# Kernel tuning notes

Measured on AMD Instinct MI355X. Metric: run time of the kernel, lower is better.

## Reference

```python
import jax, jax.numpy as jnp
import numpy as np

N_NODES = 100000
N_EDGES = 3200000
D_IN = 256
D_OUT = 256


def setup_inputs() -> dict:
    key = jax.random.key(0)
    k1, k2, k3, k4, k5 = jax.random.split(key, 5)
    x = jax.random.normal(k1, (N_NODES, D_IN), dtype=jnp.float32)
    # xavier-uniform-like init for weight
    limit = float(np.sqrt(6.0 / (D_IN + D_OUT)))
    weight = jax.random.uniform(k2, (D_IN, D_OUT), dtype=jnp.float32, minval=-limit, maxval=limit)
    edge_val = jax.random.uniform(k3, (N_EDGES,), dtype=jnp.float32)
    edge_row = jax.random.randint(k4, (N_EDGES,), 0, N_NODES, dtype=jnp.int32)
    edge_col = jax.random.randint(k5, (N_EDGES,), 0, N_NODES, dtype=jnp.int32)
    return {"x": x, "weight": weight, "edge_val": edge_val,
            "edge_row": edge_row, "edge_col": edge_col}


def reference(x, weight, edge_val, edge_row, edge_col):
    # dropout p=0.0 -> identity
    support = x @ weight                                  # [N, D_OUT]
    # spmm: out[r] += val * support[c] for each edge (r, c, val)
    msgs = support[edge_col] * edge_val[:, None]          # [E, D_OUT]
    out = jax.ops.segment_sum(msgs, edge_row, num_segments=N_NODES)
    return jax.nn.relu(out)
```

## Files before the change

### kernel.cpp

```cpp
#include <hip/hip_runtime.h>

#define N_NODES 100000
#define N_EDGES 3200000
#define D 256
#define OVF_MAX 8192

#define RPB 256
#define NBUCK 391
#define CAPB 11264

#define CHUNK 4096
#define NBLK_A ((N_EDGES + CHUNK - 1) / CHUNK)

#define GEMM_BLOCKS (N_NODES / 16)
#define SCAP 9216

typedef __attribute__((ext_vector_type(8))) short bf16x8;
typedef __attribute__((ext_vector_type(4))) float f32x4;
typedef __attribute__((ext_vector_type(2))) float f32x2;

__device__ unsigned short g_wtp[(size_t)16 * 8 * 64 * 8];
__device__ unsigned short g_support[(size_t)N_NODES * D];
__device__ int   g_bucket_cur[NBUCK];
__device__ int2  g_binned[(size_t)NBUCK * CAPB];
__device__ int   g_novf;
__device__ int   g_ovf_row[OVF_MAX];
__device__ int2  g_ovf_edge[OVF_MAX];

__device__ __forceinline__ unsigned short f2bf(float f) {
    unsigned u = __float_as_uint(f);
    unsigned r = u + 0x7fffu + ((u >> 16) & 1u);
    return (unsigned short)(r >> 16);
}

__global__ void setup_kernel(const float* __restrict__ W) {
    const int tid = threadIdx.x;
    if (blockIdx.x < 64) {
        int pb = (blockIdx.x * 256 + tid) * 4;
        #pragma unroll
        for (int j = 0; j < 4; ++j) {
            int p    = pb + j;
            int i8   = p & 7;
            int lane = (p >> 3) & 63;
            int s    = (p >> 9) & 7;
            int nt   = p >> 12;
            int n = nt * 16 + (lane & 15);
            int k = s * 32 + (lane >> 4) * 8 + i8;
            g_wtp[p] = f2bf(W[(size_t)k * D + n]);
        }
    }
    for (int i = blockIdx.x * blockDim.x + tid; i < NBUCK;
         i += gridDim.x * blockDim.x)
        g_bucket_cur[i] = 0;
    if (blockIdx.x == 0 && tid == 0) g_novf = 0;
}

union SmemK2 {
    struct {
        int2 rec[CHUNK];
        int  cnt[NBUCK];
        int  pre[NBUCK + 1];
        int  bas[NBUCK];
    } bin;
    float tile[4][16][68];
};

__launch_bounds__(256)
__global__ void bin_gemm_kernel(const float* __restrict__ x,
                                const float* __restrict__ edge_val,
                                const int* __restrict__ edge_row,
                                const int* __restrict__ edge_col) {
    __shared__ SmemK2 sm;
    const int tid = threadIdx.x;
    const int b = blockIdx.x;

    if (b < NBLK_A) {
        auto& B = sm.bin;
        const int e0 = b * CHUNK;
        for (int q = tid; q < NBUCK; q += 256) B.cnt[q] = 0;
        __syncthreads();
        #pragma unroll
        for (int j = 0; j < CHUNK / 256; ++j) {
            int e = e0 + tid + j * 256;
            if (e < N_EDGES) atomicAdd(&B.cnt[edge_row[e] >> 8], 1);
        }
        __syncthreads();
        if (tid == 0) {
            int run = 0;
            for (int q = 0; q < NBUCK; ++q) { B.pre[q] = run; run += B.cnt[q]; }
            B.pre[NBUCK] = run;
        }
        __syncthreads();
        for (int q = tid; q < NBUCK; q += 256)
            B.bas[q] = B.cnt[q] ? atomicAdd(&g_bucket_cur[q], B.cnt[q]) : 0;
        __syncthreads();
        for (int q = tid; q < NBUCK; q += 256) B.cnt[q] = 0;
        __syncthreads();
        #pragma unroll
        for (int j = 0; j < CHUNK / 256; ++j) {
            int e = e0 + tid + j * 256;
            if (e < N_EDGES) {
                int r = edge_row[e];
                int q = r >> 8;
                int o = atomicAdd(&B.cnt[q], 1);
                int2 pk;
                pk.x = edge_col[e] | ((r & 255) << 17);
                pk.y = __float_as_int(edge_val[e]);
                B.rec[B.pre[q] + o] = pk;
            }
        }
        __syncthreads();
        const int total = B.pre[NBUCK];
        for (int i = tid; i < total; i += 256) {
            int lo = 0, hi = NBUCK;
            while (hi - lo > 1) {
                int mid = (lo + hi) >> 1;
                if (B.pre[mid] <= i) lo = mid; else hi = mid;
            }
            int q = lo;
            int dest = B.bas[q] + (i - B.pre[q]);
            int2 pk = B.rec[i];
            if (dest < CAPB) {
                g_binned[(size_t)q * CAPB + dest] = pk;
            } else {
                int o = atomicAdd(&g_novf, 1);
                if (o < OVF_MAX) {
                    g_ovf_row[o] = (q << 8) | (pk.x >> 17);
                    int2 ov; ov.x = pk.x & 0x1FFFF; ov.y = pk.y;
                    g_ovf_edge[o] = ov;
                }
            }
        }
    } else {
        const int g    = b - NBLK_A;
        const int wave = tid >> 6;
        const int lane = tid & 63;
        const int m0   = g * 16;
        const int n0   = wave * 64;
        const int lm   = lane & 15;
        const int q    = lane >> 4;

        f32x4 acc0 = {}, acc1 = {}, acc2 = {}, acc3 = {};

        #pragma unroll
        for (int s = 0; s < 8; ++s) {
            const int k0 = s * 32;
            const float* Arow = &x[(size_t)(m0 + lm) * D + k0 + q * 8];
            float4 f0 = *(const float4*)&Arow[0];
            float4 f1 = *(const float4*)&Arow[4];
            union { bf16x8 v; unsigned short u[8]; } au;
            au.u[0] = f2bf(f0.x); au.u[1] = f2bf(f0.y);
            au.u[2] = f2bf(f0.z); au.u[3] = f2bf(f0.w);
            au.u[4] = f2bf(f1.x); au.u[5] = f2bf(f1.y);
            au.u[6] = f2bf(f1.z); au.u[7] = f2bf(f1.w);

            const unsigned short* bp =
                &g_wtp[((size_t)(wave * 4) * 8 + s) * 512 + lane * 8];
            bf16x8 b0 = *(const bf16x8*)&bp[0 * 4096];
            bf16x8 b1 = *(const bf16x8*)&bp[1 * 4096];
            bf16x8 b2 = *(const bf16x8*)&bp[2 * 4096];
            bf16x8 b3 = *(const bf16x8*)&bp[3 * 4096];
            acc0 = __builtin_amdgcn_mfma_f32_16x16x32_bf16(au.v, b0, acc0, 0, 0, 0);
            acc1 = __builtin_amdgcn_mfma_f32_16x16x32_bf16(au.v, b1, acc1, 0, 0, 0);
            acc2 = __builtin_amdgcn_mfma_f32_16x16x32_bf16(au.v, b2, acc2, 0, 0, 0);
            acc3 = __builtin_amdgcn_mfma_f32_16x16x32_bf16(au.v, b3, acc3, 0, 0, 0);
        }

        #pragma unroll
        for (int r = 0; r < 4; ++r) {
            sm.tile[wave][q * 4 + r][ 0 + lm] = acc0[r];
            sm.tile[wave][q * 4 + r][16 + lm] = acc1[r];
            sm.tile[wave][q * 4 + r][32 + lm] = acc2[r];
            sm.tile[wave][q * 4 + r][48 + lm] = acc3[r];
        }
        const int row  = lane >> 2;
        const int cseg = (lane & 3) * 16;
        unsigned short outv[16];
        #pragma unroll
        for (int j = 0; j < 16; ++j)
            outv[j] = f2bf(sm.tile[wave][row][cseg + j]);
        unsigned short* dst = &g_support[(size_t)(m0 + row) * D + n0 + cseg];
        *(uint4*)&dst[0] = *(const uint4*)&outv[0];
        *(uint4*)&dst[8] = *(const uint4*)&outv[8];
    }
}

__launch_bounds__(1024)
__global__ void spmm_kernel(float* __restrict__ out) {
    __shared__ int2 srec[SCAP];
    __shared__ int rcnt[RPB];
    __shared__ int rofs[RPB];
    __shared__ int rcur[RPB];
    const int k   = blockIdx.x;
    const int tid = threadIdx.x;
    const int nrec_all = min(g_bucket_cur[k], CAPB);
    const int nstage   = min(nrec_all, SCAP);
    const int2* src = &g_binned[(size_t)k * CAPB];

    for (int i = tid; i < RPB; i += 1024) { rcnt[i] = 0; rcur[i] = 0; }
    __syncthreads();
    for (int i = tid; i < nstage; i += 1024)
        atomicAdd(&rcnt[src[i].x >> 17], 1);
    __syncthreads();
    if (tid < RPB) {
        int s = 0;
        for (int j = 0; j < tid; ++j) s += rcnt[j];
        rofs[tid] = s;
    }
    __syncthreads();
    for (int i = tid; i < nstage; i += 1024) {
        int2 pk = src[i];
        int rl  = pk.x >> 17;
        int pos = rofs[rl] + atomicAdd(&rcur[rl], 1);
        srec[pos] = pk;
    }
    __syncthreads();

    const int grp = tid >> 7;
    const int t   = tid & 127;
    const unsigned* sup = (const unsigned*)g_support;
    const int novf = min(g_novf, OVF_MAX);

    for (int rr = 0; rr < 32; ++rr) {
        const int rl  = grp * 32 + rr;
        const int row = (k << 8) + rl;
        if (row >= N_NODES) break;
        const int cnt = rcnt[rl];
        const int ofs = rofs[rl];
        float a0 = 0.f, a1 = 0.f;
        int i = 0;
        for (; i + 3 < cnt; i += 4) {
            int2 e0 = srec[ofs + i];
            int2 e1 = srec[ofs + i + 1];
            int2 e2 = srec[ofs + i + 2];
            int2 e3 = srec[ofs + i + 3];
            unsigned p0 = sup[(size_t)(e0.x & 0x1FFFF) * (D / 2) + t];
            unsigned p1 = sup[(size_t)(e1.x & 0x1FFFF) * (D / 2) + t];
            unsigned p2 = sup[(size_t)(e2.x & 0x1FFFF) * (D / 2) + t];
            unsigned p3 = sup[(size_t)(e3.x & 0x1FFFF) * (D / 2) + t];
            float v0 = __int_as_float(e0.y);
            float v1 = __int_as_float(e1.y);
            float v2 = __int_as_float(e2.y);
            float v3 = __int_as_float(e3.y);
            a0 += v0 * __uint_as_float(p0 << 16);
            a1 += v0 * __uint_as_float(p0 & 0xffff0000u);
            a0 += v1 * __uint_as_float(p1 << 16);
            a1 += v1 * __uint_as_float(p1 & 0xffff0000u);
            a0 += v2 * __uint_as_float(p2 << 16);
            a1 += v2 * __uint_as_float(p2 & 0xffff0000u);
            a0 += v3 * __uint_as_float(p3 << 16);
            a1 += v3 * __uint_as_float(p3 & 0xffff0000u);
        }
        for (; i < cnt; ++i) {
            int2 e0 = srec[ofs + i];
            unsigned p0 = sup[(size_t)(e0.x & 0x1FFFF) * (D / 2) + t];
            float v0 = __int_as_float(e0.y);
            a0 += v0 * __uint_as_float(p0 << 16);
            a1 += v0 * __uint_as_float(p0 & 0xffff0000u);
        }
        for (int j = nstage; j < nrec_all; ++j) {
            int2 pk = src[j];
            if ((pk.x >> 17) == rl) {
                unsigned p0 = sup[(size_t)(pk.x & 0x1FFFF) * (D / 2) + t];
                float v0 = __int_as_float(pk.y);
                a0 += v0 * __uint_as_float(p0 << 16);
                a1 += v0 * __uint_as_float(p0 & 0xffff0000u);
            }
        }
        if (novf > 0) {
            for (int j = 0; j < novf; ++j) {
                if (g_ovf_row[j] == row) {
                    int2 ee = g_ovf_edge[j];
                    float v0 = __int_as_float(ee.y);
                    unsigned p0 = sup[(size_t)ee.x * (D / 2) + t];
                    a0 += v0 * __uint_as_float(p0 << 16);
                    a1 += v0 * __uint_as_float(p0 & 0xffff0000u);
                }
            }
        }
        f32x2 o;
        o.x = fmaxf(a0, 0.f);
        o.y = fmaxf(a1, 0.f);
        __builtin_nontemporal_store(o, (f32x2*)&out[(size_t)row * D + 2 * t]);
    }
}

extern "C" void kernel_launch(void* const* d_in, const int* in_sizes, int n_in,
                              void* d_out, int out_size, void* d_ws, size_t ws_size,
                              hipStream_t stream) {
    const float* x        = (const float*)d_in[0];
    const float* weight   = (const float*)d_in[1];
    const float* edge_val = (const float*)d_in[2];
    const int*   edge_row = (const int*)d_in[3];
    const int*   edge_col = (const int*)d_in[4];
    float* out = (float*)d_out;

    setup_kernel<<<64, 256, 0, stream>>>(weight);
    bin_gemm_kernel<<<NBLK_A + GEMM_BLOCKS, 256, 0, stream>>>(x, edge_val, edge_row, edge_col);
    spmm_kernel<<<NBUCK, 1024, 0, stream>>>(out);
}
```

Measured before the change: 607.1 us.

## Reorder to aggregate-then-transform: SpMM on bf16 x, then GEMM with fused ReLU

The product is reassociated so the sparse aggregation runs on a bf16 copy of x first, and the dense weight GEMM runs afterwards on the aggregated bf16 result, with ReLU fused into the GEMM epilogue. The GEMM no longer writes an intermediate support matrix; instead a cast kernel writes bf16 x and spmm writes a bf16 intermediate. Buckets shrink to 128 rows with 782 blocks of 512 threads, and a per-record bucket id replaces the binary search in the scatter phase. This adds one kernel launch and an extra bf16 rounding of the aggregated sums, which may change accuracy.

```diff
diff --git a/kernel.cpp b/kernel.cpp
--- a/kernel.cpp
+++ b/kernel.cpp
@@ -5,22 +5,24 @@
 #define D 256
 #define OVF_MAX 8192
 
-#define RPB 256
-#define NBUCK 391
-#define CAPB 11264
+#define RPB 128
+#define NBUCK 782
+#define CAPB 5120
+#define SCAP 4608
 
 #define CHUNK 4096
 #define NBLK_A ((N_EDGES + CHUNK - 1) / CHUNK)
-
+#define NGRP 196
+
+#define CAST_BLOCKS 6250
 #define GEMM_BLOCKS (N_NODES / 16)
-#define SCAP 9216
 
 typedef __attribute__((ext_vector_type(8))) short bf16x8;
 typedef __attribute__((ext_vector_type(4))) float f32x4;
-typedef __attribute__((ext_vector_type(2))) float f32x2;
 
 __device__ unsigned short g_wtp[(size_t)16 * 8 * 64 * 8];
-__device__ unsigned short g_support[(size_t)N_NODES * D];
+__device__ unsigned short g_xb[(size_t)N_NODES * D];
+__device__ unsigned       g_y[(size_t)N_NODES * (D / 2)];
 __device__ int   g_bucket_cur[NBUCK];
 __device__ int2  g_binned[(size_t)NBUCK * CAPB];
 __device__ int   g_novf;
@@ -55,138 +57,103 @@
     if (blockIdx.x == 0 && tid == 0) g_novf = 0;
 }
 
-union SmemK2 {
-    struct {
-        int2 rec[CHUNK];
-        int  cnt[NBUCK];
-        int  pre[NBUCK + 1];
-        int  bas[NBUCK];
-    } bin;
-    float tile[4][16][68];
-};
-
 __launch_bounds__(256)
-__global__ void bin_gemm_kernel(const float* __restrict__ x,
+__global__ void bin_cast_kernel(const float* __restrict__ x,
                                 const float* __restrict__ edge_val,
                                 const int* __restrict__ edge_row,
                                 const int* __restrict__ edge_col) {
-    __shared__ SmemK2 sm;
+    __shared__ int2 rec[CHUNK];
+    __shared__ unsigned short bid[CHUNK];
+    __shared__ int cnt[NGRP * 4];
+    __shared__ int pre[NBUCK + 1];
+    __shared__ int bas[NBUCK];
+    __shared__ int gs[NGRP];
+    __shared__ int gofs[NGRP];
     const int tid = threadIdx.x;
     const int b = blockIdx.x;
 
     if (b < NBLK_A) {
-        auto& B = sm.bin;
         const int e0 = b * CHUNK;
-        for (int q = tid; q < NBUCK; q += 256) B.cnt[q] = 0;
+        for (int q = tid; q < NGRP * 4; q += 256) cnt[q] = 0;
         __syncthreads();
         #pragma unroll
         for (int j = 0; j < CHUNK / 256; ++j) {
             int e = e0 + tid + j * 256;
-            if (e < N_EDGES) atomicAdd(&B.cnt[edge_row[e] >> 8], 1);
-        }
-        __syncthreads();
-        if (tid == 0) {
-            int run = 0;
-            for (int q = 0; q < NBUCK; ++q) { B.pre[q] = run; run += B.cnt[q]; }
-            B.pre[NBUCK] = run;
-        }
+            if (e < N_EDGES) atomicAdd(&cnt[edge_row[e] >> 7], 1);
+        }
+        __syncthreads();
+        if (tid < NGRP) {
+            const int* c = &cnt[tid * 4];
+            gs[tid] = c[0] + c[1] + c[2] + c[3];
+        }
+        __syncthreads();
+        if (tid < NGRP) {
+            int s = 0;
+            for (int j = 0; j < tid; ++j) s += gs[j];
+            gofs[tid] = s;
+        }
+        __syncthreads();
+        for (int q = tid; q < NBUCK; q += 256) {
+            int p = gofs[q >> 2];
+            for (int j = q & ~3; j < q; ++j) p += cnt[j];
+            pre[q] = p;
+        }
+        if (tid == 0) pre[NBUCK] = gofs[NGRP - 1] + gs[NGRP - 1];
         __syncthreads();
         for (int q = tid; q < NBUCK; q += 256)
-            B.bas[q] = B.cnt[q] ? atomicAdd(&g_bucket_cur[q], B.cnt[q]) : 0;
-        __syncthreads();
-        for (int q = tid; q < NBUCK; q += 256) B.cnt[q] = 0;
+            bas[q] = cnt[q] ? atomicAdd(&g_bucket_cur[q], cnt[q]) : 0;
+        __syncthreads();
+        for (int q = tid; q < NGRP * 4; q += 256) cnt[q] = 0;
         __syncthreads();
         #pragma unroll
         for (int j = 0; j < CHUNK / 256; ++j) {
             int e = e0 + tid + j * 256;
             if (e < N_EDGES) {
                 int r = edge_row[e];
-                int q = r >> 8;
-                int o = atomicAdd(&B.cnt[q], 1);
+                int q = r >> 7;
+                int o = atomicAdd(&cnt[q], 1);
+                int pos = pre[q] + o;
                 int2 pk;
-                pk.x = edge_col[e] | ((r & 255) << 17);
+                pk.x = edge_col[e] | ((r & 127) << 17);
                 pk.y = __float_as_int(edge_val[e]);
-                B.rec[B.pre[q] + o] = pk;
+                rec[pos] = pk;
+                bid[pos] = (unsigned short)q;
             }
         }
         __syncthreads();
-        const int total = B.pre[NBUCK];
+        const int total = pre[NBUCK];
         for (int i = tid; i < total; i += 256) {
-            int lo = 0, hi = NBUCK;
-            while (hi - lo > 1) {
-                int mid = (lo + hi) >> 1;
-                if (B.pre[mid] <= i) lo = mid; else hi = mid;
-            }
-            int q = lo;
-            int dest = B.bas[q] + (i - B.pre[q]);
-            int2 pk = B.rec[i];
+            int q = bid[i];
+            int dest = bas[q] + (i - pre[q]);
+            int2 pk = rec[i];
             if (dest < CAPB) {
                 g_binned[(size_t)q * CAPB + dest] = pk;
             } else {
                 int o = atomicAdd(&g_novf, 1);
                 if (o < OVF_MAX) {
-                    g_ovf_row[o] = (q << 8) | (pk.x >> 17);
+                    g_ovf_row[o] = (q << 7) | (pk.x >> 17);
                     int2 ov; ov.x = pk.x & 0x1FFFF; ov.y = pk.y;
                     g_ovf_edge[o] = ov;
                 }
             }
         }
     } else {
-        const int g    = b - NBLK_A;
-        const int wave = tid >> 6;
-        const int lane = tid & 63;
-        const int m0   = g * 16;
-        const int n0   = wave * 64;
-        const int lm   = lane & 15;
-        const int q    = lane >> 4;
-
-        f32x4 acc0 = {}, acc1 = {}, acc2 = {}, acc3 = {};
-
-        #pragma unroll
-        for (int s = 0; s < 8; ++s) {
-            const int k0 = s * 32;
-            const float* Arow = &x[(size_t)(m0 + lm) * D + k0 + q * 8];
-            float4 f0 = *(const float4*)&Arow[0];
-            float4 f1 = *(const float4*)&Arow[4];
-            union { bf16x8 v; unsigned short u[8]; } au;
-            au.u[0] = f2bf(f0.x); au.u[1] = f2bf(f0.y);
-            au.u[2] = f2bf(f0.z); au.u[3] = f2bf(f0.w);
-            au.u[4] = f2bf(f1.x); au.u[5] = f2bf(f1.y);
-            au.u[6] = f2bf(f1.z); au.u[7] = f2bf(f1.w);
-
-            const unsigned short* bp =
-                &g_wtp[((size_t)(wave * 4) * 8 + s) * 512 + lane * 8];
-            bf16x8 b0 = *(const bf16x8*)&bp[0 * 4096];
-            bf16x8 b1 = *(const bf16x8*)&bp[1 * 4096];
-            bf16x8 b2 = *(const bf16x8*)&bp[2 * 4096];
-            bf16x8 b3 = *(const bf16x8*)&bp[3 * 4096];
-            acc0 = __builtin_amdgcn_mfma_f32_16x16x32_bf16(au.v, b0, acc0, 0, 0, 0);
-            acc1 = __builtin_amdgcn_mfma_f32_16x16x32_bf16(au.v, b1, acc1, 0, 0, 0);
-            acc2 = __builtin_amdgcn_mfma_f32_16x16x32_bf16(au.v, b2, acc2, 0, 0, 0);
-            acc3 = __builtin_amdgcn_mfma_f32_16x16x32_bf16(au.v, b3, acc3, 0, 0, 0);
-        }
-
-        #pragma unroll
-        for (int r = 0; r < 4; ++r) {
-            sm.tile[wave][q * 4 + r][ 0 + lm] = acc0[r];
-            sm.tile[wave][q * 4 + r][16 + lm] = acc1[r];
-            sm.tile[wave][q * 4 + r][32 + lm] = acc2[r];
-            sm.tile[wave][q * 4 + r][48 + lm] = acc3[r];
-        }
-        const int row  = lane >> 2;
-        const int cseg = (lane & 3) * 16;
-        unsigned short outv[16];
-        #pragma unroll
-        for (int j = 0; j < 16; ++j)
-            outv[j] = f2bf(sm.tile[wave][row][cseg + j]);
-        unsigned short* dst = &g_support[(size_t)(m0 + row) * D + n0 + cseg];
-        *(uint4*)&dst[0] = *(const uint4*)&outv[0];
-        *(uint4*)&dst[8] = *(const uint4*)&outv[8];
-    }
-}
-
-__launch_bounds__(1024)
-__global__ void spmm_kernel(float* __restrict__ out) {
+        const size_t base = (size_t)(b - NBLK_A) * 4096 + (size_t)tid * 16;
+        const float4* xp = (const float4*)&x[base];
+        float4 f0 = xp[0], f1 = xp[1], f2 = xp[2], f3 = xp[3];
+        unsigned short o[16];
+        o[ 0]=f2bf(f0.x); o[ 1]=f2bf(f0.y); o[ 2]=f2bf(f0.z); o[ 3]=f2bf(f0.w);
+        o[ 4]=f2bf(f1.x); o[ 5]=f2bf(f1.y); o[ 6]=f2bf(f1.z); o[ 7]=f2bf(f1.w);
+        o[ 8]=f2bf(f2.x); o[ 9]=f2bf(f2.y); o[10]=f2bf(f2.z); o[11]=f2bf(f2.w);
+        o[12]=f2bf(f3.x); o[13]=f2bf(f3.y); o[14]=f2bf(f3.z); o[15]=f2bf(f3.w);
+        uint4* dst = (uint4*)&g_xb[base];
+        dst[0] = *(const uint4*)&o[0];
+        dst[1] = *(const uint4*)&o[8];
+    }
+}
+
+__launch_bounds__(512)
+__global__ void spmm_kernel() {
     __shared__ int2 srec[SCAP];
     __shared__ int rcnt[RPB];
     __shared__ int rofs[RPB];
@@ -197,9 +164,9 @@
     const int nstage   = min(nrec_all, SCAP);
     const int2* src = &g_binned[(size_t)k * CAPB];
 
-    for (int i = tid; i < RPB; i += 1024) { rcnt[i] = 0; rcur[i] = 0; }
+    if (tid < RPB) { rcnt[tid] = 0; rcur[tid] = 0; }
     __syncthreads();
-    for (int i = tid; i < nstage; i += 1024)
+    for (int i = tid; i < nstage; i += 512)
         atomicAdd(&rcnt[src[i].x >> 17], 1);
     __syncthreads();
     if (tid < RPB) {
@@ -208,7 +175,7 @@
         rofs[tid] = s;
     }
     __syncthreads();
-    for (int i = tid; i < nstage; i += 1024) {
+    for (int i = tid; i < nstage; i += 512) {
         int2 pk = src[i];
         int rl  = pk.x >> 17;
         int pos = rofs[rl] + atomicAdd(&rcur[rl], 1);
@@ -218,12 +185,12 @@
 
     const int grp = tid >> 7;
     const int t   = tid & 127;
-    const unsigned* sup = (const unsigned*)g_support;
+    const unsigned* xb = (const unsigned*)g_xb;
     const int novf = min(g_novf, OVF_MAX);
 
     for (int rr = 0; rr < 32; ++rr) {
         const int rl  = grp * 32 + rr;
-        const int row = (k << 8) + rl;
+        const int row = k * RPB + rl;
         if (row >= N_NODES) break;
         const int cnt = rcnt[rl];
         const int ofs = rofs[rl];
@@ -234,10 +201,10 @@
             int2 e1 = srec[ofs + i + 1];
             int2 e2 = srec[ofs + i + 2];
             int2 e3 = srec[ofs + i + 3];
-            unsigned p0 = sup[(size_t)(e0.x & 0x1FFFF) * (D / 2) + t];
-            unsigned p1 = sup[(size_t)(e1.x & 0x1FFFF) * (D / 2) + t];
-            unsigned p2 = sup[(size_t)(e2.x & 0x1FFFF) * (D / 2) + t];
-            unsigned p3 = sup[(size_t)(e3.x & 0x1FFFF) * (D / 2) + t];
+            unsigned p0 = xb[(size_t)(e0.x & 0x1FFFF) * (D / 2) + t];
+            unsigned p1 = xb[(size_t)(e1.x & 0x1FFFF) * (D / 2) + t];
+            unsigned p2 = xb[(size_t)(e2.x & 0x1FFFF) * (D / 2) + t];
+            unsigned p3 = xb[(size_t)(e3.x & 0x1FFFF) * (D / 2) + t];
             float v0 = __int_as_float(e0.y);
             float v1 = __int_as_float(e1.y);
             float v2 = __int_as_float(e2.y);
@@ -253,7 +220,7 @@
         }
         for (; i < cnt; ++i) {
             int2 e0 = srec[ofs + i];
-            unsigned p0 = sup[(size_t)(e0.x & 0x1FFFF) * (D / 2) + t];
+            unsigned p0 = xb[(size_t)(e0.x & 0x1FFFF) * (D / 2) + t];
             float v0 = __int_as_float(e0.y);
             a0 += v0 * __uint_as_float(p0 << 16);
             a1 += v0 * __uint_as_float(p0 & 0xffff0000u);
@@ -261,7 +228,7 @@
         for (int j = nstage; j < nrec_all; ++j) {
             int2 pk = src[j];
             if ((pk.x >> 17) == rl) {
-                unsigned p0 = sup[(size_t)(pk.x & 0x1FFFF) * (D / 2) + t];
+                unsigned p0 = xb[(size_t)(pk.x & 0x1FFFF) * (D / 2) + t];
                 float v0 = __int_as_float(pk.y);
                 a0 += v0 * __uint_as_float(p0 << 16);
                 a1 += v0 * __uint_as_float(p0 & 0xffff0000u);
@@ -272,17 +239,63 @@
                 if (g_ovf_row[j] == row) {
                     int2 ee = g_ovf_edge[j];
                     float v0 = __int_as_float(ee.y);
-                    unsigned p0 = sup[(size_t)ee.x * (D / 2) + t];
+                    unsigned p0 = xb[(size_t)ee.x * (D / 2) + t];
                     a0 += v0 * __uint_as_float(p0 << 16);
                     a1 += v0 * __uint_as_float(p0 & 0xffff0000u);
                 }
             }
         }
-        f32x2 o;
-        o.x = fmaxf(a0, 0.f);
-        o.y = fmaxf(a1, 0.f);
-        __builtin_nontemporal_store(o, (f32x2*)&out[(size_t)row * D + 2 * t]);
-    }
+        g_y[(size_t)row * (D / 2) + t] =
+            (unsigned)f2bf(a0) | ((unsigned)f2bf(a1) << 16);
+    }
+}
+
+__launch_bounds__(256)
+__global__ void gemm_kernel(float* __restrict__ out) {
+    __shared__ float tile[4][16][68];
+    const int g    = blockIdx.x;
+    const int wave = threadIdx.x >> 6;
+    const int lane = threadIdx.x & 63;
+    const int m0   = g * 16;
+    const int n0   = wave * 64;
+    const int lm   = lane & 15;
+    const int q    = lane >> 4;
+
+    const unsigned short* Yb = (const unsigned short*)g_y;
+    f32x4 acc0 = {}, acc1 = {}, acc2 = {}, acc3 = {};
+
+    #pragma unroll
+    for (int s = 0; s < 8; ++s) {
+        bf16x8 av = *(const bf16x8*)&Yb[(size_t)(m0 + lm) * D + s * 32 + q * 8];
+        const unsigned short* bp =
+            &g_wtp[((size_t)(wave * 4) * 8 + s) * 512 + lane * 8];
+        bf16x8 b0 = *(const bf16x8*)&bp[0 * 4096];
+        bf16x8 b1 = *(const bf16x8*)&bp[1 * 4096];
+        bf16x8 b2 = *(const bf16x8*)&bp[2 * 4096];
+        bf16x8 b3 = *(const bf16x8*)&bp[3 * 4096];
+        acc0 = __builtin_amdgcn_mfma_f32_16x16x32_bf16(av, b0, acc0, 0, 0, 0);
+        acc1 = __builtin_amdgcn_mfma_f32_16x16x32_bf16(av, b1, acc1, 0, 0, 0);
+        acc2 = __builtin_amdgcn_mfma_f32_16x16x32_bf16(av, b2, acc2, 0, 0, 0);
+        acc3 = __builtin_amdgcn_mfma_f32_16x16x32_bf16(av, b3, acc3, 0, 0, 0);
+    }
+
+    #pragma unroll
+    for (int r = 0; r < 4; ++r) {
+        tile[wave][q * 4 + r][ 0 + lm] = acc0[r];
+        tile[wave][q * 4 + r][16 + lm] = acc1[r];
+        tile[wave][q * 4 + r][32 + lm] = acc2[r];
+        tile[wave][q * 4 + r][48 + lm] = acc3[r];
+    }
+    const int row  = lane >> 2;
+    const int cseg = (lane & 3) * 16;
+    float ov[16];
+    #pragma unroll
+    for (int j = 0; j < 16; ++j)
+        ov[j] = fmaxf(tile[wave][row][cseg + j], 0.f);
+    float* dst = &out[(size_t)(m0 + row) * D + n0 + cseg];
+    #pragma unroll
+    for (int j = 0; j < 4; ++j)
+        __builtin_nontemporal_store(*(const f32x4*)&ov[j * 4], (f32x4*)&dst[j * 4]);
 }
 
 extern "C" void kernel_launch(void* const* d_in, const int* in_sizes, int n_in,
@@ -296,6 +309,7 @@
     float* out = (float*)d_out;
 
     setup_kernel<<<64, 256, 0, stream>>>(weight);
-    bin_gemm_kernel<<<NBLK_A + GEMM_BLOCKS, 256, 0, stream>>>(x, edge_val, edge_row, edge_col);
-    spmm_kernel<<<NBUCK, 1024, 0, stream>>>(out);
-}
+    bin_cast_kernel<<<NBLK_A + CAST_BLOCKS, 256, 0, stream>>>(x, edge_val, edge_row, edge_col);
+    spmm_kernel<<<NBUCK, 512, 0, stream>>>();
+    gemm_kernel<<<GEMM_BLOCKS, 256, 0, stream>>>(out);
+}
```

Result: slower. 655.8 us (+8.0%).
